# Optimization experiments

Hardware: AMD Instinct MI355X
Metric: run time of the kernel (lower is better)

The kernel has to match this reference:

```python
import jax, jax.numpy as jnp
import numpy as np

STRIDES = (8.0, 16.0, 32.0)
SCORE_T = 0.25
NMS_T = 0.45
DET = 100          # max detections per image
PRE_NMS = 1000     # static top-k surrogate for torch.where score filtering
MAX_SIZE = 4096.0  # class offset for batched (class-aware) NMS
IMG = 640.0        # image side (square), used for box clamping
ANCHORS = np.array([[[10,13],[16,30],[33,23]],
                    [[30,61],[62,45],[59,119]],
                    [[116,90],[156,198],[373,326]]], dtype=np.float32)


def setup_inputs() -> dict:
    key = jax.random.key(0)
    k0, k1, k2 = jax.random.split(key, 3)
    return {
        "pred0": jax.random.normal(k0, (16, 80, 80, 3, 85), dtype=jnp.float32),
        "pred1": jax.random.normal(k1, (16, 40, 40, 3, 85), dtype=jnp.float32),
        "pred2": jax.random.normal(k2, (16, 20, 20, 3, 85), dtype=jnp.float32),
        "anchors": jnp.asarray(ANCHORS),
        "scale_factors": jnp.ones((16,), dtype=jnp.float32),
    }


def _decode_level(pred, stride, anc):
    # pred: [B,H,W,A,5+C], anc: [A,2]
    p = jax.nn.sigmoid(pred)
    B, H, W, A, E = p.shape
    C = E - 5
    gx, gy = jnp.meshgrid(jnp.arange(W, dtype=p.dtype),
                          jnp.arange(H, dtype=p.dtype), indexing='xy')
    grid = jnp.stack((gx, gy), -1)                      # [H,W,2] = (x,y)
    xy = (2.0 * p[..., :2] - 0.5 + grid[None, :, :, None, :]) * stride
    wh = 4.0 * jnp.square(p[..., 2:4]) * anc            # [B,H,W,A,2]
    boxes = jnp.concatenate((xy - wh * 0.5, xy + wh * 0.5), -1)  # cxcywh->xyxy
    obj = p[..., 4:5]
    s = obj * p[..., 5:]                                # [B,H,W,A,C]
    s = jnp.where((obj > SCORE_T) & (s > SCORE_T), s, 0.0)
    return boxes.reshape(B, -1, 4), s.reshape(B, -1, C)


def _box_iou_1n(box, boxes):
    # box [4], boxes [K,4] -> iou [K]
    lt = jnp.maximum(box[:2], boxes[:, :2])
    rb = jnp.minimum(box[2:], boxes[:, 2:])
    wh = jnp.clip(rb - lt, 0.0)
    inter = wh[:, 0] * wh[:, 1]
    a1 = (box[2] - box[0]) * (box[3] - box[1])
    a2 = (boxes[:, 2] - boxes[:, 0]) * (boxes[:, 3] - boxes[:, 1])
    return inter / (a1 + a2 - inter + 1e-7)


def _per_image(boxes, scores, scale):
    # boxes [M,4], scores [M,C]
    C = scores.shape[-1]
    topv, topi = jax.lax.top_k(scores.reshape(-1), PRE_NMS)
    bidx = topi // C
    lab = topi % C
    bx = boxes[bidx]                                    # [K,4]
    obx = bx + lab.astype(bx.dtype)[:, None] * MAX_SIZE  # class-offset boxes

    def body(i, st):
        sc, keep, ks = st
        j = jnp.argmax(sc)
        keep = keep.at[i].set(j)
        ks = ks.at[i].set(sc[j])
        iou = _box_iou_1n(obx[j], obx)
        sc = jnp.where(iou > NMS_T, 0.0, sc)
        return sc, keep, ks

    st0 = (topv, jnp.zeros((DET,), jnp.int32), jnp.zeros((DET,), bx.dtype))
    _, keep, ks = jax.lax.fori_loop(0, DET, body, st0)
    kb = bx[keep] / scale
    kl = lab[keep].astype(bx.dtype)
    valid = ks > 0
    kb = jnp.where(valid[:, None], kb, 0.0)
    kl = jnp.where(valid, kl, -1.0)
    return jnp.concatenate((kb, ks[:, None], kl[:, None]), -1)  # [DET,6]


def reference(pred0, pred1, pred2, anchors, scale_factors):
    preds = (pred0, pred1, pred2)
    bs, ss = [], []
    for lvl, (pred, stride) in enumerate(zip(preds, STRIDES)):
        b, s = _decode_level(pred, stride, anchors[lvl])
        bs.append(b)
        ss.append(s)
    boxes = jnp.clip(jnp.concatenate(bs, 1), 0.0, IMG)   # [B,M,4]
    scores = jnp.concatenate(ss, 1)                      # [B,M,C]
    return jax.vmap(_per_image)(boxes, scores, scale_factors)  # [B,DET,6]
```

## Files before the change

kernel.cpp:

```cpp
#include <hip/hip_runtime.h>
#include <cstdint>
#include <cstddef>

#pragma clang fp contract(off)

constexpr int NIMG  = 16;
constexpr int NB0   = 19200;
constexpr int NB1   = 4800;
constexpr int NB2   = 1200;
constexpr int NBOX  = 25200;
constexpr int NCLS  = 80;
constexpr int NCH   = 85;
constexpr int NBINS = 4096;
constexpr int CAP   = 4096;
constexpr int NTOP  = 1000;
constexpr int NDET  = 100;
constexpr float IMGSZ = 640.0f;
constexpr float BIN_SCALE = 4096.0f / 0.75f;

constexpr int TILE    = 128;
constexpr int TILES   = (NBOX + TILE - 1) / TILE;

constexpr int IOU_RPB = 40;
constexpr int LOWBIN  = 2000;
constexpr float LUMP_S = 0.25f + (float)LOWBIN / BIN_SCALE;

typedef float float4a __attribute__((ext_vector_type(4), aligned(4)));
typedef float float2a __attribute__((ext_vector_type(2), aligned(4)));

__device__ __forceinline__ float xla_expf(float x) {
  const float kLog2e = 1.44269504088896341f;
  const float kC1 = 0.693359375f;
  const float kC2 = -2.12194440e-4f;
  const float cp0 = 1.9875691500e-4f;
  const float cp1 = 1.3981999507e-3f;
  const float cp2 = 8.3334519073e-3f;
  const float cp3 = 4.1665795894e-2f;
  const float cp4 = 1.6666665459e-1f;
  const float cp5 = 5.0000001201e-1f;
  float xc = fminf(x, 88.3762626647950f);
  xc = fmaxf(xc, -88.3762626647949f);
  float fx = floorf(fmaf(xc, kLog2e, 0.5f));
  float xr = fmaf(fx, -kC1, xc);
  xr = fmaf(fx, -kC2, xr);
  float z = xr * xr;
  float y = fmaf(cp0, xr, cp1);
  y = fmaf(y, xr, cp2);
  y = fmaf(y, xr, cp3);
  y = fmaf(y, xr, cp4);
  y = fmaf(y, xr, cp5);
  y = fmaf(y, z, xr);
  y = y + 1.0f;
  int n = (int)fx;
  float two_n = __int_as_float((n + 127) << 23);
  float r = y * two_n;
  return fmaxf(r, xc);
}

__device__ __forceinline__ float ref_sigmoid(float x) {
  return 1.0f / (1.0f + xla_expf(-x));
}

__device__ __forceinline__ float fast_sigmoid(float x) {
  float e = __expf(-x);
  return __fdividef(1.0f, 1.0f + e);
}

__device__ __forceinline__ int score_bin(float s) {
  int b = (int)((s - 0.25f) * BIN_SCALE);
  return min(max(b, 0), NBINS - 1);
}

__device__ __forceinline__ const float* locate(int img, int box,
    const float* __restrict__ p0, const float* __restrict__ p1, const float* __restrict__ p2,
    int& lvl, int& gx, int& gy, int& anc, float& stride) {
  const float* base; int r, W;
  if (box < NB0)            { lvl = 0; r = box;             W = 80; base = p0 + (size_t)img * NB0 * NCH; stride = 8.0f;  }
  else if (box < NB0 + NB1) { lvl = 1; r = box - NB0;       W = 40; base = p1 + (size_t)img * NB1 * NCH; stride = 16.0f; }
  else                      { lvl = 2; r = box - NB0 - NB1; W = 20; base = p2 + (size_t)img * NB2 * NCH; stride = 32.0f; }
  anc = r % 3;
  int cell = r / 3;
  gx = cell % W;
  gy = cell / W;
  return base + (size_t)r * NCH;
}

__device__ __forceinline__ float clip640(float v) {
  return fminf(fmaxf(v, 0.0f), IMGSZ);
}

__device__ __forceinline__ const float* row_ptr(int img, int box,
    const float* __restrict__ p0, const float* __restrict__ p1, const float* __restrict__ p2) {
  const float* base; int r;
  if (box < NB0)            { base = p0 + (size_t)img * NB0 * NCH; r = box; }
  else if (box < NB0 + NB1) { base = p1 + (size_t)img * NB1 * NCH; r = box - NB0; }
  else                      { base = p2 + (size_t)img * NB2 * NCH; r = box - NB0 - NB1; }
  return base + (size_t)r * NCH;
}

__global__ __launch_bounds__(256) void k_passA(const float* __restrict__ p0,
    const float* __restrict__ p1, const float* __restrict__ p2,
    unsigned int* __restrict__ ghist, unsigned short* __restrict__ maxbin) {
  __shared__ unsigned int hist[NBINS];
  const int tid = threadIdx.x;
  const int img  = blockIdx.x / TILES;
  const int tile = blockIdx.x % TILES;
  const int tbase = tile * TILE;
  const int nbox_tile = min(TILE, NBOX - tbase);
  const int lane = tid & 63;

  for (int i = tid; i < NBINS; i += 256) hist[i] = 0u;
  __syncthreads();

  const int b_local = tid >> 3, part = tid & 7;
  int lowc = 0;

  float   xoR[2];
  float4a vaR[2], vbR[2];
  float2a vcR[2];

#define PA_ISSUE(SLOT, STEP) do {                                   \
    int bl_ = (STEP) * 32 + b_local;                                \
    int box_ = tbase + min(bl_, nbox_tile - 1);                     \
    const float* row_ = row_ptr(img, box_, p0, p1, p2);             \
    xoR[SLOT] = row_[4];                                            \
    const float* cls_ = row_ + 5 + 10 * part;                       \
    vaR[SLOT] = *(const float4a*)(cls_);                            \
    vbR[SLOT] = *(const float4a*)(cls_ + 4);                        \
    vcR[SLOT] = *(const float2a*)(cls_ + 8);                        \
  } while (0)

  PA_ISSUE(0, 0);
  #pragma unroll
  for (int step = 0; step < TILE / 32; ++step) {
    const int cur = step & 1;
    if (step + 1 < TILE / 32) PA_ISSUE((step + 1) & 1, step + 1);

    int bl = step * 32 + b_local;
    bool valid = (bl < nbox_tile);
    float xo = xoR[cur];
    float v[10] = { vaR[cur].x, vaR[cur].y, vaR[cur].z, vaR[cur].w,
                    vbR[cur].x, vbR[cur].y, vbR[cur].z, vbR[cur].w,
                    vcR[cur].x, vcR[cur].y };

    float obj = 0.0f, tcons = 3.0e38f, thi = 3.0e38f;
    if (part == 0) {
      obj = fast_sigmoid(xo);
      if (valid && obj > 0.2499f) {
        float rr = 0.2499f / obj;
        tcons = __logf(__fdividef(rr, 1.0f - rr)) - 0.05f;
        float rh = LUMP_S / obj;
        if (rh < 1.0f) thi = __logf(__fdividef(rh, 1.0f - rh)) - 0.05f;
      }
    }
    obj   = __shfl(obj,   0, 8);
    tcons = __shfl(tcons, 0, 8);
    thi   = __shfl(thi,   0, 8);

    int mb = 0;
    #pragma unroll
    for (int k = 0; k < 10; ++k) {
      float x = v[k];
      if (x > tcons) {
        if (x > thi) {
          float s = obj * fast_sigmoid(x);
          if (s > 0.2499f) {
            int bin = score_bin(s);
            atomicAdd(&hist[bin], 1u);
            mb = max(mb, bin + 1);
          }
        } else {
          ++lowc;
          mb = max(mb, LOWBIN);
        }
      }
    }
    mb = max(mb, __shfl_xor(mb, 1, 8));
    mb = max(mb, __shfl_xor(mb, 2, 8));
    mb = max(mb, __shfl_xor(mb, 4, 8));
    if (valid && part == 0)
      maxbin[(size_t)img * NBOX + tbase + bl] = (unsigned short)mb;
  }
#undef PA_ISSUE

  #pragma unroll
  for (int d = 1; d < 64; d <<= 1) lowc += __shfl_xor(lowc, d);
  if (lane == 0 && lowc) atomicAdd(&hist[0], (unsigned int)lowc);
  __syncthreads();

  for (int i = tid; i < NBINS; i += 256) {
    unsigned int v2 = hist[i];
    if (v2) atomicAdd(&ghist[img * NBINS + i], v2);
  }
}

__global__ __launch_bounds__(256) void k_thresh(const unsigned int* __restrict__ ghist,
                                                int* __restrict__ tbin) {
  __shared__ unsigned int h[NBINS];
  __shared__ unsigned int psum[256];
  const int tid = threadIdx.x;
  const int img = blockIdx.x;

  for (int i = tid; i < NBINS; i += 256) h[i] = ghist[img * NBINS + i];
  __syncthreads();
  unsigned int ps = 0;
  for (int k = 0; k < 16; ++k) ps += h[tid * 16 + k];
  psum[tid] = ps;
  __syncthreads();
  if (tid == 0) {
    long long cum = 0;
    int tb = 0;
    bool found = false;
    for (int g = 255; g >= 0 && !found; --g) {
      if (cum + (long long)psum[g] >= NTOP) {
        for (int b = g * 16 + 15; b >= g * 16; --b) {
          cum += h[b];
          if (cum >= NTOP) { tb = b; found = true; break; }
        }
      } else {
        cum += psum[g];
      }
    }
    if (!found) tb = 0;
    int tc = (tb >= 2) ? tb - 2 : 0;
    for (int b = tb - 1; b >= tc; --b) cum += h[b];
    while (cum > CAP - 8 && tc < NBINS - 1) { cum -= h[tc]; ++tc; }
    tbin[img] = tc;
  }
}

__global__ __launch_bounds__(256) void k_wlemit(const float* __restrict__ p0,
    const float* __restrict__ p1, const float* __restrict__ p2,
    const unsigned short* __restrict__ maxbin, const int* __restrict__ tbin,
    unsigned long long* __restrict__ cand, int* __restrict__ cnt) {
  __shared__ unsigned int list[256];
  __shared__ int lcnt;
  const int tid = threadIdx.x;
  const int lane = tid & 63;
  if (tid == 0) lcnt = 0;
  __syncthreads();

  int idx = blockIdx.x * 256 + tid;
  if (idx < NIMG * NBOX) {
    int img = idx / NBOX;
    int box = idx - img * NBOX;
    if ((int)maxbin[idx] > tbin[img])
      list[atomicAdd(&lcnt, 1)] = ((unsigned int)img << 16) | (unsigned int)box;
  }
  __syncthreads();
  const int n = lcnt;
  const int nsweep = (n + 31) / 32;

  for (int s = 0; s < nsweep; ++s) {
    int r = s * 32 + (tid >> 3);
    int part = tid & 7;
    bool have = (r < n);
    int img = 0, box = 0, nc = 0;
    unsigned int bm = 0;
    float obj_e = -1.0f;
    float v[10];
    if (have) {
      unsigned int e = list[r];
      img = (int)(e >> 16);
      box = (int)(e & 0xFFFFu);
      const float* row = row_ptr(img, box, p0, p1, p2);
      float xo = row[4];
      float obj_f = fast_sigmoid(xo);
      if (obj_f > 0.2499f) {
        const float* cls = row + 5 + 10 * part;
        float4a va = *(const float4a*)(cls);
        float4a vb = *(const float4a*)(cls + 4);
        float2a vc = *(const float2a*)(cls + 8);
        v[0]=va.x; v[1]=va.y; v[2]=va.z; v[3]=va.w;
        v[4]=vb.x; v[5]=vb.y; v[6]=vb.z; v[7]=vb.w;
        v[8]=vc.x; v[9]=vc.y;
        int tc = tbin[img];
        #pragma unroll
        for (int k = 0; k < 10; ++k) {
          float sf = obj_f * fast_sigmoid(v[k]);
          if (sf > 0.2499f && score_bin(sf) >= tc) {
            if (obj_e < 0.0f) obj_e = ref_sigmoid(xo);
            if (obj_e > 0.25f) {
              float se = obj_e * ref_sigmoid(v[k]);
              if (se > 0.25f) { bm |= 1u << k; ++nc; }
            }
          }
        }
      }
    }

    int mybase = 0;
    unsigned long long active = __ballot(nc > 0);
    while (active) {
      int leader = __ffsll(active) - 1;
      int limg = __shfl(img, leader);
      bool mine = (nc > 0) && (img == limg);
      unsigned long long grp = __ballot(mine);
      int incl = mine ? nc : 0;
      #pragma unroll
      for (int d = 1; d < 64; d <<= 1) {
        int t = __shfl_up(incl, d);
        if (lane >= d) incl += t;
      }
      int hi = 63 - __clzll(grp);
      int total = __shfl(incl, hi);
      int base = 0;
      if (lane == leader) base = atomicAdd(&cnt[limg], total);
      base = __shfl(base, leader);
      if (mine) mybase = base + incl - nc;
      active &= ~grp;
    }

    if (nc > 0) {
      int pos = mybase;
      #pragma unroll
      for (int k = 0; k < 10; ++k) {
        if (bm & (1u << k)) {
          float se = obj_e * ref_sigmoid(v[k]);
          if (pos < CAP) {
            unsigned int fi = (unsigned int)(box * NCLS + 10 * part + k);
            unsigned long long key =
                ((unsigned long long)__float_as_uint(se) << 32) |
                (unsigned long long)(0xFFFFFFFFu - fi);
            cand[(size_t)img * CAP + pos] = key;
          }
          ++pos;
        }
      }
    }
  }
}

#define SIDX(i) ((i) + ((i) >> 4))

__global__ __launch_bounds__(1024) void k_sort(const float* __restrict__ p0,
    const float* __restrict__ p1, const float* __restrict__ p2,
    const float* __restrict__ anchors, const unsigned long long* __restrict__ cand,
    const int* __restrict__ cnt_arr, float* __restrict__ boxes8) {
  __shared__ unsigned long long keys[CAP + CAP / 16];
  __shared__ int n2_sh, cnt_sh;
  const int tid = threadIdx.x;
  const int img = blockIdx.x;

  if (tid == 0) {
    int c = cnt_arr[img];
    c = max(0, min(c, CAP));
    int n2 = 1024;
    while (n2 < c) n2 <<= 1;
    cnt_sh = c; n2_sh = n2;
  }
  __syncthreads();
  const int cnt = cnt_sh;
  const int n2  = n2_sh;

  const unsigned long long* c = cand + (size_t)img * CAP;
  for (int i = tid; i < n2; i += 1024) keys[SIDX(i)] = (i < cnt) ? c[i] : 0ull;
  __syncthreads();

  for (int kk = 2; kk <= n2; kk <<= 1) {
    for (int j = kk >> 1; j > 0; j >>= 1) {
      for (int i = tid; i < n2; i += 1024) {
        int l = i ^ j;
        if (l > i) {
          unsigned long long a = keys[SIDX(i)], b = keys[SIDX(l)];
          bool up = ((i & kk) == 0);
          bool sw = up ? (a < b) : (a > b);
          if (sw) { keys[SIDX(i)] = b; keys[SIDX(l)] = a; }
        }
      }
      __syncthreads();
    }
  }

  float* dst = boxes8 + (size_t)img * NTOP * 8;
  if (tid < NTOP) {
    int i = tid;
    unsigned long long key = keys[SIDX(i)];
    unsigned int v = (unsigned int)(key >> 32);
    float4 fa, fb;
    if (v) {
      unsigned int idx = 0xFFFFFFFFu - (unsigned int)(key & 0xFFFFFFFFu);
      int box = (int)(idx / NCLS);
      int l   = (int)(idx % NCLS);
      int lvl, gx, gy, anc; float stride;
      const float* ptr = locate(img, box, p0, p1, p2, lvl, gx, gy, anc, stride);
      float sx = ref_sigmoid(ptr[0]);
      float sy = ref_sigmoid(ptr[1]);
      float sw = ref_sigmoid(ptr[2]);
      float sh = ref_sigmoid(ptr[3]);
      float aw = anchors[(lvl * 3 + anc) * 2 + 0];
      float ah = anchors[(lvl * 3 + anc) * 2 + 1];
      float cx = (2.0f * sx - 0.5f + (float)gx) * stride;
      float cy = (2.0f * sy - 0.5f + (float)gy) * stride;
      float ww = (4.0f * (sw * sw)) * aw;
      float hh = (4.0f * (sh * sh)) * ah;
      fa.x = clip640(cx - ww * 0.5f);
      fa.y = clip640(cy - hh * 0.5f);
      fa.z = clip640(cx + ww * 0.5f);
      fa.w = clip640(cy + hh * 0.5f);
      fb.x = __uint_as_float(v);
      fb.y = (float)l;
      fb.z = 0.0f; fb.w = 0.0f;
    } else {
      fa.x = fa.y = fa.z = fa.w = 0.0f;
      fb.x = 0.0f; fb.y = -1.0f; fb.z = 0.0f; fb.w = 0.0f;
    }
    *(float4*)(dst + i * 8)     = fa;
    *(float4*)(dst + i * 8 + 4) = fb;
  }
}

__global__ __launch_bounds__(256) void k_iou(const float* __restrict__ boxes8,
                                             unsigned int* __restrict__ mat) {
  __shared__ float obx[NTOP * 5];
  const int img = blockIdx.x / (NTOP / IOU_RPB);
  const int rg  = blockIdx.x % (NTOP / IOU_RPB);
  const float* src = boxes8 + (size_t)img * NTOP * 8;

  for (int t = threadIdx.x; t < NTOP; t += 256) {
    float4 fa = *(const float4*)(src + t * 8);
    float lab = src[t * 8 + 5];
    float off = lab * 4096.0f;
    obx[t * 5 + 0] = fa.x + off;
    obx[t * 5 + 1] = fa.y + off;
    obx[t * 5 + 2] = fa.z + off;
    obx[t * 5 + 3] = fa.w + off;
  }
  __syncthreads();

  const int wave = threadIdx.x >> 6;
  const int lane = threadIdx.x & 63;
  for (int task = wave; task < IOU_RPB * 16; task += 4) {
    int r = rg * IOU_RPB + (task >> 4);
    int w = task & 15;
    float a0 = obx[r * 5 + 0], a1 = obx[r * 5 + 1];
    float a2 = obx[r * 5 + 2], a3 = obx[r * 5 + 3];
    float areaA = (a2 - a0) * (a3 - a1);
    int col = w * 64 + lane;
    bool bit = false;
    if (col < NTOP) {
      float o0 = obx[col * 5 + 0], o1 = obx[col * 5 + 1];
      float o2 = obx[col * 5 + 2], o3 = obx[col * 5 + 3];
      float ltx = fmaxf(a0, o0);
      float lty = fmaxf(a1, o1);
      float rbx = fminf(a2, o2);
      float rby = fminf(a3, o3);
      float wx = fmaxf(rbx - ltx, 0.0f);
      float wy = fmaxf(rby - lty, 0.0f);
      float inter = wx * wy;
      float a2r = (o2 - o0) * (o3 - o1);
      float denom = areaA + a2r - inter + 1e-7f;
      bit = (inter / denom) > 0.45f;
    }
    unsigned long long m = __ballot(bit);
    if (lane == 0)
      *(unsigned long long*)(mat + ((size_t)img * NTOP + r) * 32 + w * 2) = m;
  }
}

__global__ __launch_bounds__(256) void k_nms(const unsigned int* __restrict__ mat,
    const float* __restrict__ boxes8, const float* __restrict__ scalef,
    float* __restrict__ out) {
  __shared__ uint4 mat_lds4[NTOP * 8];
  unsigned int* mat_lds = (unsigned int*)mat_lds4;
  const int tid = threadIdx.x;
  const int lane = tid & 63;
  const int img = blockIdx.x;
  const float* src = boxes8 + (size_t)img * NTOP * 8;

  const uint4* msrc = (const uint4*)(mat + (size_t)img * NTOP * 32);
  for (int i = tid; i < NTOP * 8; i += 256) mat_lds4[i] = msrc[i];
  __syncthreads();
  if (tid >= 64) return;

  unsigned int aw = 0u;
  for (int w = 0; w < 16; ++w) {
    int t = w * 64 + lane;
    float va = (t < NTOP) ? src[t * 8 + 4] : 0.0f;
    unsigned long long b = __ballot(va > 0.0f);
    if (lane == 2 * w)     aw = (unsigned int)b;
    if (lane == 2 * w + 1) aw = (unsigned int)(b >> 32);
  }
  if (lane >= 32) aw = 0u;

  int pj0 = -1, pj1 = -1;
  for (int i = 0; i < NDET; ++i) {
    unsigned long long bal = __ballot(aw != 0u);
    int j = -1;
    if (bal != 0ull) {
      int L = __ffsll(bal) - 1;
      unsigned int wL = (unsigned int)__shfl((int)aw, L);
      j = L * 32 + (__ffs(wL) - 1);
    }
    if (lane == (i & 63)) { if (i < 64) pj0 = j; else pj1 = j; }
    if (j >= 0 && lane < 32) aw &= ~mat_lds[j * 32 + lane];
  }

  const float scf = scalef[img];
  #pragma unroll
  for (int rep = 0; rep < 2; ++rep) {
    int i = rep * 64 + lane;
    if (i >= NDET) break;
    int j = (rep == 0) ? pj0 : pj1;
    float* orow = out + ((size_t)img * NDET + i) * 6;
    if (j < 0) {
      orow[0] = 0.0f; orow[1] = 0.0f; orow[2] = 0.0f;
      orow[3] = 0.0f; orow[4] = 0.0f; orow[5] = -1.0f;
    } else {
      float4 fa = *(const float4*)(src + j * 8);
      float va = src[j * 8 + 4];
      float lb = src[j * 8 + 5];
      orow[0] = fa.x / scf; orow[1] = fa.y / scf;
      orow[2] = fa.z / scf; orow[3] = fa.w / scf;
      orow[4] = va;
      orow[5] = lb;
    }
  }
}

extern "C" void kernel_launch(void* const* d_in, const int* in_sizes, int n_in,
                              void* d_out, int out_size, void* d_ws, size_t ws_size,
                              hipStream_t stream) {
  const float* p0 = (const float*)d_in[0];
  const float* p1 = (const float*)d_in[1];
  const float* p2 = (const float*)d_in[2];
  const float* anchors = (const float*)d_in[3];
  const float* scalef  = (const float*)d_in[4];
  float* out = (float*)d_out;

  char* w = (char*)d_ws;
  unsigned int* ghist = (unsigned int*)(w);
  int* cnt  = (int*)(w + 262144);
  int* tbin = (int*)(w + 262208);
  unsigned long long* cand = (unsigned long long*)(w + 262336);
  unsigned short* maxbin = (unsigned short*)(w + 262336 + 524288);
  float* boxes8 = (float*)(w + 786624 + 806400 + 64);
  unsigned int* mat = (unsigned int*)(w + 1593088 + 512000);

  hipMemsetAsync(ghist, 0, 262144 + 192, stream);

  k_passA<<<dim3(NIMG * TILES), dim3(256), 0, stream>>>(p0, p1, p2, ghist, maxbin);
  k_thresh<<<dim3(NIMG), dim3(256), 0, stream>>>(ghist, tbin);
  k_wlemit<<<dim3((NIMG * NBOX + 255) / 256), dim3(256), 0, stream>>>(p0, p1, p2, maxbin, tbin, cand, cnt);
  k_sort<<<dim3(NIMG), dim3(1024), 0, stream>>>(p0, p1, p2, anchors, cand, cnt, boxes8);
  k_iou<<<dim3(NIMG * (NTOP / IOU_RPB)), dim3(256), 0, stream>>>(boxes8, mat);
  k_nms<<<dim3(NIMG), dim3(256), 0, stream>>>(mat, boxes8, scalef, out);
}
```

Baseline: 179.4 us.

## Fuse threshold, candidate emit and sort into one per-image kernel

Merges the histogram-threshold, candidate-emission and bitonic-sort kernels into a single 1024-thread block per image. Candidates are written straight into shared-memory sort keys, so the global candidate buffer, the count array and two kernel launches go away. In exchange the emit phase, which used to spread over about 1,500 blocks across the GPU, now runs on only 16 blocks. It scans maxbin in chunks with several barriers each, so that phase becomes latency-bound.

```diff
diff --git a/kernel.cpp b/kernel.cpp
--- a/kernel.cpp
+++ b/kernel.cpp
@@ -24,6 +24,7 @@
 constexpr int IOU_RPB = 40;
 constexpr int LOWBIN  = 2000;
 constexpr float LUMP_S = 0.25f + (float)LOWBIN / BIN_SCALE;
+constexpr int CHUNKB  = 2048;
 
 typedef float float4a __attribute__((ext_vector_type(4), aligned(4)));
 typedef float float2a __attribute__((ext_vector_type(2), aligned(4)));
@@ -194,18 +195,27 @@
   }
 }
 
-__global__ __launch_bounds__(256) void k_thresh(const unsigned int* __restrict__ ghist,
-                                                int* __restrict__ tbin) {
-  __shared__ unsigned int h[NBINS];
+#define SIDX(i) ((i) + ((i) >> 4))
+
+__global__ __launch_bounds__(1024) void k_fuse(const float* __restrict__ p0,
+    const float* __restrict__ p1, const float* __restrict__ p2,
+    const float* __restrict__ anchors, const unsigned int* __restrict__ ghist,
+    const unsigned short* __restrict__ maxbin, float* __restrict__ boxes8) {
+  __shared__ unsigned long long keys[CAP + CAP / 16];
+  __shared__ unsigned int list[CHUNKB];
   __shared__ unsigned int psum[256];
+  __shared__ int tc_sh, kcnt, lcnt, n2_sh, c_sh;
   const int tid = threadIdx.x;
   const int img = blockIdx.x;
 
-  for (int i = tid; i < NBINS; i += 256) h[i] = ghist[img * NBINS + i];
-  __syncthreads();
-  unsigned int ps = 0;
-  for (int k = 0; k < 16; ++k) ps += h[tid * 16 + k];
-  psum[tid] = ps;
+  unsigned int* h = (unsigned int*)keys;
+  for (int i = tid; i < NBINS; i += 1024) h[i] = ghist[img * NBINS + i];
+  __syncthreads();
+  if (tid < 256) {
+    unsigned int ps = 0;
+    for (int k = 0; k < 16; ++k) ps += h[tid * 16 + k];
+    psum[tid] = ps;
+  }
   __syncthreads();
   if (tid == 0) {
     long long cum = 0;
@@ -225,136 +235,76 @@
     int tc = (tb >= 2) ? tb - 2 : 0;
     for (int b = tb - 1; b >= tc; --b) cum += h[b];
     while (cum > CAP - 8 && tc < NBINS - 1) { cum -= h[tc]; ++tc; }
-    tbin[img] = tc;
-  }
-}
-
-__global__ __launch_bounds__(256) void k_wlemit(const float* __restrict__ p0,
-    const float* __restrict__ p1, const float* __restrict__ p2,
-    const unsigned short* __restrict__ maxbin, const int* __restrict__ tbin,
-    unsigned long long* __restrict__ cand, int* __restrict__ cnt) {
-  __shared__ unsigned int list[256];
-  __shared__ int lcnt;
-  const int tid = threadIdx.x;
-  const int lane = tid & 63;
-  if (tid == 0) lcnt = 0;
-  __syncthreads();
-
-  int idx = blockIdx.x * 256 + tid;
-  if (idx < NIMG * NBOX) {
-    int img = idx / NBOX;
-    int box = idx - img * NBOX;
-    if ((int)maxbin[idx] > tbin[img])
-      list[atomicAdd(&lcnt, 1)] = ((unsigned int)img << 16) | (unsigned int)box;
-  }
-  __syncthreads();
-  const int n = lcnt;
-  const int nsweep = (n + 31) / 32;
-
-  for (int s = 0; s < nsweep; ++s) {
-    int r = s * 32 + (tid >> 3);
-    int part = tid & 7;
-    bool have = (r < n);
-    int img = 0, box = 0, nc = 0;
-    unsigned int bm = 0;
-    float obj_e = -1.0f;
-    float v[10];
-    if (have) {
-      unsigned int e = list[r];
-      img = (int)(e >> 16);
-      box = (int)(e & 0xFFFFu);
-      const float* row = row_ptr(img, box, p0, p1, p2);
-      float xo = row[4];
-      float obj_f = fast_sigmoid(xo);
-      if (obj_f > 0.2499f) {
-        const float* cls = row + 5 + 10 * part;
-        float4a va = *(const float4a*)(cls);
-        float4a vb = *(const float4a*)(cls + 4);
-        float2a vc = *(const float2a*)(cls + 8);
-        v[0]=va.x; v[1]=va.y; v[2]=va.z; v[3]=va.w;
-        v[4]=vb.x; v[5]=vb.y; v[6]=vb.z; v[7]=vb.w;
-        v[8]=vc.x; v[9]=vc.y;
-        int tc = tbin[img];
-        #pragma unroll
-        for (int k = 0; k < 10; ++k) {
-          float sf = obj_f * fast_sigmoid(v[k]);
-          if (sf > 0.2499f && score_bin(sf) >= tc) {
-            if (obj_e < 0.0f) obj_e = ref_sigmoid(xo);
-            if (obj_e > 0.25f) {
-              float se = obj_e * ref_sigmoid(v[k]);
-              if (se > 0.25f) { bm |= 1u << k; ++nc; }
+    tc_sh = tc;
+    kcnt = 0;
+  }
+  __syncthreads();
+  const int tc = tc_sh;
+
+  for (int base = 0; base < NBOX; base += CHUNKB) {
+    __syncthreads();
+    if (tid == 0) lcnt = 0;
+    __syncthreads();
+    #pragma unroll
+    for (int q = 0; q < CHUNKB / 1024; ++q) {
+      int b = base + q * 1024 + tid;
+      if (b < NBOX && (int)maxbin[(size_t)img * NBOX + b] > tc)
+        list[atomicAdd(&lcnt, 1)] = (unsigned int)b;
+    }
+    __syncthreads();
+    const int ln = lcnt;
+
+    for (int s0 = 0; s0 < ln; s0 += 128) {
+      int r = s0 + (tid >> 3);
+      int part = tid & 7;
+      if (r < ln) {
+        int box = (int)list[r];
+        const float* row = row_ptr(img, box, p0, p1, p2);
+        float xo = row[4];
+        float obj_f = fast_sigmoid(xo);
+        if (obj_f > 0.2499f) {
+          const float* cls = row + 5 + 10 * part;
+          float4a va = *(const float4a*)(cls);
+          float4a vb = *(const float4a*)(cls + 4);
+          float2a vc = *(const float2a*)(cls + 8);
+          float v[10] = { va.x, va.y, va.z, va.w, vb.x, vb.y, vb.z, vb.w, vc.x, vc.y };
+          float obj_e = -1.0f;
+          #pragma unroll
+          for (int k = 0; k < 10; ++k) {
+            float sf = obj_f * fast_sigmoid(v[k]);
+            if (sf > 0.2499f && score_bin(sf) >= tc) {
+              if (obj_e < 0.0f) obj_e = ref_sigmoid(xo);
+              if (obj_e > 0.25f) {
+                float se = obj_e * ref_sigmoid(v[k]);
+                if (se > 0.25f) {
+                  int pos = atomicAdd(&kcnt, 1);
+                  if (pos < CAP) {
+                    unsigned int fi = (unsigned int)(box * NCLS + 10 * part + k);
+                    unsigned long long key =
+                        ((unsigned long long)__float_as_uint(se) << 32) |
+                        (unsigned long long)(0xFFFFFFFFu - fi);
+                    keys[SIDX(pos)] = key;
+                  }
+                }
+              }
             }
           }
         }
       }
     }
-
-    int mybase = 0;
-    unsigned long long active = __ballot(nc > 0);
-    while (active) {
-      int leader = __ffsll(active) - 1;
-      int limg = __shfl(img, leader);
-      bool mine = (nc > 0) && (img == limg);
-      unsigned long long grp = __ballot(mine);
-      int incl = mine ? nc : 0;
-      #pragma unroll
-      for (int d = 1; d < 64; d <<= 1) {
-        int t = __shfl_up(incl, d);
-        if (lane >= d) incl += t;
-      }
-      int hi = 63 - __clzll(grp);
-      int total = __shfl(incl, hi);
-      int base = 0;
-      if (lane == leader) base = atomicAdd(&cnt[limg], total);
-      base = __shfl(base, leader);
-      if (mine) mybase = base + incl - nc;
-      active &= ~grp;
-    }
-
-    if (nc > 0) {
-      int pos = mybase;
-      #pragma unroll
-      for (int k = 0; k < 10; ++k) {
-        if (bm & (1u << k)) {
-          float se = obj_e * ref_sigmoid(v[k]);
-          if (pos < CAP) {
-            unsigned int fi = (unsigned int)(box * NCLS + 10 * part + k);
-            unsigned long long key =
-                ((unsigned long long)__float_as_uint(se) << 32) |
-                (unsigned long long)(0xFFFFFFFFu - fi);
-            cand[(size_t)img * CAP + pos] = key;
-          }
-          ++pos;
-        }
-      }
-    }
-  }
-}
-
-#define SIDX(i) ((i) + ((i) >> 4))
-
-__global__ __launch_bounds__(1024) void k_sort(const float* __restrict__ p0,
-    const float* __restrict__ p1, const float* __restrict__ p2,
-    const float* __restrict__ anchors, const unsigned long long* __restrict__ cand,
-    const int* __restrict__ cnt_arr, float* __restrict__ boxes8) {
-  __shared__ unsigned long long keys[CAP + CAP / 16];
-  __shared__ int n2_sh, cnt_sh;
-  const int tid = threadIdx.x;
-  const int img = blockIdx.x;
+  }
+  __syncthreads();
 
   if (tid == 0) {
-    int c = cnt_arr[img];
-    c = max(0, min(c, CAP));
+    int c = min(kcnt, CAP);
     int n2 = 1024;
     while (n2 < c) n2 <<= 1;
-    cnt_sh = c; n2_sh = n2;
-  }
-  __syncthreads();
-  const int cnt = cnt_sh;
-  const int n2  = n2_sh;
-
-  const unsigned long long* c = cand + (size_t)img * CAP;
-  for (int i = tid; i < n2; i += 1024) keys[SIDX(i)] = (i < cnt) ? c[i] : 0ull;
+    c_sh = c; n2_sh = n2;
+  }
+  __syncthreads();
+  const int c = c_sh;
+  const int n2 = n2_sh;
+  for (int i = c + tid; i < n2; i += 1024) keys[SIDX(i)] = 0ull;
   __syncthreads();
 
   for (int kk = 2; kk <= n2; kk <<= 1) {
@@ -530,19 +480,14 @@
 
   char* w = (char*)d_ws;
   unsigned int* ghist = (unsigned int*)(w);
-  int* cnt  = (int*)(w + 262144);
-  int* tbin = (int*)(w + 262208);
-  unsigned long long* cand = (unsigned long long*)(w + 262336);
-  unsigned short* maxbin = (unsigned short*)(w + 262336 + 524288);
-  float* boxes8 = (float*)(w + 786624 + 806400 + 64);
-  unsigned int* mat = (unsigned int*)(w + 1593088 + 512000);
-
-  hipMemsetAsync(ghist, 0, 262144 + 192, stream);
+  unsigned short* maxbin = (unsigned short*)(w + 262144);
+  float* boxes8 = (float*)(w + 262144 + 806400);
+  unsigned int* mat = (unsigned int*)(w + 1068544 + 512000);
+
+  hipMemsetAsync(ghist, 0, 262144, stream);
 
   k_passA<<<dim3(NIMG * TILES), dim3(256), 0, stream>>>(p0, p1, p2, ghist, maxbin);
-  k_thresh<<<dim3(NIMG), dim3(256), 0, stream>>>(ghist, tbin);
-  k_wlemit<<<dim3((NIMG * NBOX + 255) / 256), dim3(256), 0, stream>>>(p0, p1, p2, maxbin, tbin, cand, cnt);
-  k_sort<<<dim3(NIMG), dim3(1024), 0, stream>>>(p0, p1, p2, anchors, cand, cnt, boxes8);
+  k_fuse<<<dim3(NIMG), dim3(1024), 0, stream>>>(p0, p1, p2, anchors, ghist, maxbin, boxes8);
   k_iou<<<dim3(NIMG * (NTOP / IOU_RPB)), dim3(256), 0, stream>>>(boxes8, mat);
   k_nms<<<dim3(NIMG), dim3(256), 0, stream>>>(mat, boxes8, scalef, out);
 }
```

Measured after the change: 210.5 us. +17.3%, slower.
